# Kernel optimization log

Hardware: AMD Instinct MI355X
Metric: run time of the kernel (lower is better)

Reference implementation:

```python
import jax, jax.numpy as jnp
import numpy as np

D_MODEL = 256
NHEAD = 8
D_HEAD = D_MODEL // NHEAD
DIM_FF = 1024
B, L = 4, 16384
LN_EPS = 1e-5


def _layernorm(x, g, b):
    mu = jnp.mean(x, axis=-1, keepdims=True)
    var = jnp.mean((x - mu) ** 2, axis=-1, keepdims=True)
    return (x - mu) * jax.lax.rsqrt(var + LN_EPS) * g + b


def _phi(x):
    # elu(x) + 1
    return jnp.where(x > 0, x + 1.0, jnp.exp(x))


def setup_inputs() -> dict:
    key = jax.random.key(0)
    ks = jax.random.split(key, 16)
    s_in = 1.0 / np.sqrt(D_MODEL)
    s_ff = 1.0 / np.sqrt(DIM_FF)
    inp = {
        "x": jax.random.normal(ks[0], (B, L, D_MODEL), dtype=jnp.float32),
        "Wq": jax.random.normal(ks[1], (D_MODEL, D_MODEL), dtype=jnp.float32) * s_in,
        "bq": jnp.zeros((D_MODEL,), jnp.float32),
        "Wk": jax.random.normal(ks[2], (D_MODEL, D_MODEL), dtype=jnp.float32) * s_in,
        "bk": jnp.zeros((D_MODEL,), jnp.float32),
        "Wv": jax.random.normal(ks[3], (D_MODEL, D_MODEL), dtype=jnp.float32) * s_in,
        "bv": jnp.zeros((D_MODEL,), jnp.float32),
        "Wo": jax.random.normal(ks[4], (D_MODEL, D_MODEL), dtype=jnp.float32) * s_in,
        "bo": jnp.zeros((D_MODEL,), jnp.float32),
        "W1": jax.random.normal(ks[5], (D_MODEL, DIM_FF), dtype=jnp.float32) * s_in,
        "b1": jnp.zeros((DIM_FF,), jnp.float32),
        "W2": jax.random.normal(ks[6], (DIM_FF, D_MODEL), dtype=jnp.float32) * s_ff,
        "b2": jnp.zeros((D_MODEL,), jnp.float32),
        "ln1_g": jnp.ones((D_MODEL,), jnp.float32),
        "ln1_b": jnp.zeros((D_MODEL,), jnp.float32),
        "ln2_g": jnp.ones((D_MODEL,), jnp.float32),
        "ln2_b": jnp.zeros((D_MODEL,), jnp.float32),
    }
    return inp


def reference(x, Wq, bq, Wk, bk, Wv, bv, Wo, bo, W1, b1, W2, b2, ln1_g, ln1_b, ln2_g, ln2_b):
    Bq, Lq, _ = x.shape
    q = (x @ Wq + bq).reshape(Bq, Lq, NHEAD, D_HEAD)
    k = (x @ Wk + bk).reshape(Bq, Lq, NHEAD, D_HEAD)
    v = (x @ Wv + bv).reshape(Bq, Lq, NHEAD, D_HEAD)
    q_phi = _phi(q)
    k_phi = _phi(k)
    # kv: [B, H, d, e]
    kv = jnp.einsum("blhd,blhe->bhde", k_phi, v)
    k_sum = k_phi.sum(axis=1)  # [B, H, d]
    z = 1.0 / (jnp.einsum("blhd,bhd->blh", q_phi, k_sum) + 1e-6)
    out = jnp.einsum("blhd,bhde,blh->blhe", q_phi, kv, z)
    out = out.reshape(Bq, Lq, D_MODEL) @ Wo + bo
    x = _layernorm(x + out, ln1_g, ln1_b)
    ff = jax.nn.relu(x @ W1 + b1) @ W2 + b2
    x = _layernorm(x + ff, ln2_g, ln2_b)
    return x
```

## Files before the change

### kernel.cpp

```cpp
#include <hip/hip_runtime.h>
#include <hip/hip_bf16.h>
#include <math.h>

#define NTOK   65536
#define L_SEQ  16384

typedef __bf16 bf16_t;
typedef bf16_t bf16x8 __attribute__((ext_vector_type(8)));
typedef bf16_t bf16x4 __attribute__((ext_vector_type(4)));
typedef float  f32x4  __attribute__((ext_vector_type(4)));

__device__ inline float phi_f(float x) { return x > 0.f ? x + 1.f : __expf(x); }

__device__ inline float quad_sum(float v) {
    v += __shfl_xor(v, 1);
    v += __shfl_xor(v, 2);
    v += __shfl_xor(v, 4);
    v += __shfl_xor(v, 8);
    return v;
}

__device__ inline float ld_any(const void* p, size_t i, int f32) {
    return f32 ? ((const float*)p)[i] : (float)((const bf16_t*)p)[i];
}

__device__ inline void async_copy16(const bf16_t* g, bf16_t* l) {
    __builtin_amdgcn_global_load_lds(
        (const __attribute__((address_space(1))) unsigned int*)g,
        (__attribute__((address_space(3))) unsigned int*)l, 16, 0, 0);
}

__device__ inline void stage_swz(const bf16_t* __restrict__ g, bf16_t* lds,
                                 int tid, int nslot, int ulog2, int rowstride) {
    const int umask = (1 << ulog2) - 1;
    for (int s = tid; s < nslot; s += 256) {
        int n = s >> ulog2, j = s & umask;
        int u = j ^ (n & umask);
        async_copy16(g + (size_t)n * rowstride + u * 8, lds + (size_t)s * 8);
    }
}

__device__ inline bf16x8 rd_swz(const bf16_t* lds, int n, int u, int ulog2) {
    int j = u ^ (n & ((1 << ulog2) - 1));
    return *(const bf16x8*)&lds[(((size_t)n << ulog2) + j) * 8];
}

__device__ inline void stage_w2ff(const bf16_t* __restrict__ W2_t, int ch,
                                  bf16_t* lds, int tid) {
    for (int S = tid; S < 1024; S += 256) {
        int r = S >> 3, phys = S & 7;
        int u = phys ^ (r & 7);
        int n = ((u >> 2) << 7) + r;
        int ks = u & 3;
        async_copy16(W2_t + (size_t)n * 1024 + ch * 32 + ks * 8, lds + (size_t)S * 8);
    }
}

__device__ inline bf16x8 rd_w2ff(const bf16_t* lds, int n, int quad) {
    int r = n & 127;
    int u = ((n >> 7) << 2) + quad;
    int phys = u ^ (r & 7);
    return *(const bf16x8*)&lds[(size_t)(r * 8 + phys) * 8];
}

__device__ inline void ld_afrags(const bf16_t* __restrict__ tile, int row, int q8,
                                 bf16x8 a[8]) {
#pragma unroll
    for (int kk = 0; kk < 8; ++kk)
        a[kk] = *(const bf16x8*)&tile[(size_t)row * 256 + kk * 32 + q8];
}

__global__ __launch_bounds__(256) void k_detect(const void* __restrict__ xraw,
                                                int* __restrict__ flag) {
    __shared__ int bad;
    if (threadIdx.x == 0) bad = 0;
    __syncthreads();
    const bf16_t* xb = (const bf16_t*)xraw;
    int mybad = 0;
#pragma unroll
    for (int j = 0; j < 16; ++j) {
        float v = fabsf((float)xb[threadIdx.x + 256 * j]);
        if (!(v <= 1000.f)) mybad = 1;
    }
    if (mybad) atomicOr(&bad, 1);
    __syncthreads();
    if (threadIdx.x == 0) *flag = bad;
}

__global__ __launch_bounds__(256) void k_convert(const void* __restrict__ xraw,
                                                 const int* __restrict__ flag,
                                                 bf16_t* __restrict__ xbf) {
    const int f = *flag;
    size_t i = ((size_t)blockIdx.x * 256 + threadIdx.x) * 4;
    if (f) {
        f32x4 v = *(const f32x4*)((const float*)xraw + i);
        bf16x4 o;
#pragma unroll
        for (int j = 0; j < 4; ++j) o[j] = (bf16_t)v[j];
        *(bf16x4*)&xbf[i] = o;
    } else {
        *(bf16x4*)&xbf[i] = *(const bf16x4*)((const bf16_t*)xraw + i);
    }
}

__global__ __launch_bounds__(256) void k_prep(
    const void* __restrict__ Wq, const void* __restrict__ Wk,
    const void* __restrict__ Wv, const void* __restrict__ Wo,
    const void* __restrict__ W1, const void* __restrict__ W2,
    const void* __restrict__ bq, const void* __restrict__ bk,
    const void* __restrict__ bv, const void* __restrict__ bo,
    const void* __restrict__ b1, const void* __restrict__ b2,
    const void* __restrict__ g1, const void* __restrict__ be1,
    const void* __restrict__ g2, const void* __restrict__ be2,
    const int* __restrict__ flag,
    bf16_t* __restrict__ Wqkv_t, bf16_t* __restrict__ Wo_t,
    bf16_t* __restrict__ W1_t, bf16_t* __restrict__ W2_t,
    bf16_t* __restrict__ pbuf, float* __restrict__ kvbuf) {
    const int f = *flag;
    int idx = blockIdx.x * 256 + threadIdx.x;
    if (idx < 196608) {
        int n = idx >> 8, k = idx & 255;
        float v;
        if (n < 256)      v = ld_any(Wq, k * 256 + n, f);
        else if (n < 512) v = ld_any(Wk, k * 256 + (n - 256), f);
        else              v = ld_any(Wv, k * 256 + (n - 512), f);
        Wqkv_t[idx] = (bf16_t)v;
    } else if (idx < 262144) {
        int i = idx - 196608; int n = i >> 8, k = i & 255;
        Wo_t[i] = (bf16_t)ld_any(Wo, k * 256 + n, f);
    } else if (idx < 524288) {
        int i = idx - 262144; int n = i >> 8, k = i & 255;
        W1_t[i] = (bf16_t)ld_any(W1, k * 1024 + n, f);
    } else if (idx < 786432) {
        int i = idx - 524288; int n = i >> 10, k = i & 1023;
        W2_t[i] = (bf16_t)ld_any(W2, k * 256 + n, f);
    } else if (idx < 820224) {
        kvbuf[idx - 786432] = 0.f;
    } else if (idx < 823552) {
        int i = idx - 820224;
        float v;
        if (i < 256)        v = ld_any(bq, i, f);
        else if (i < 512)   v = ld_any(bk, i - 256, f);
        else if (i < 768)   v = ld_any(bv, i - 512, f);
        else if (i < 1024)  v = ld_any(bo, i - 768, f);
        else if (i < 2048)  v = ld_any(b1, i - 1024, f);
        else if (i < 2304)  v = ld_any(b2, i - 2048, f);
        else if (i < 2560)  v = ld_any(g1, i - 2304, f);
        else if (i < 2816)  v = ld_any(be1, i - 2560, f);
        else if (i < 3072)  v = ld_any(g2, i - 2816, f);
        else                v = ld_any(be2, i - 3072, f);
        pbuf[i] = (bf16_t)v;
    }
}

__global__ __launch_bounds__(256, 4) void k_qkv(
    const bf16_t* __restrict__ x, const bf16_t* __restrict__ Wqkv_t,
    const bf16_t* __restrict__ pbuf,
    bf16_t* __restrict__ q_phi, bf16_t* __restrict__ k_phi,
    bf16_t* __restrict__ v_out) {
    const int mt = blockIdx.x, nt = blockIdx.y;
    const int tid = threadIdx.x, wave = tid >> 6, lane = tid & 63;
    const int l15 = lane & 15, quad = lane >> 4, q8 = quad * 8;
    __shared__ __align__(16) bf16_t bs[128 * 256];
    const int m0 = mt * 64;
    bf16x8 a[8];
    ld_afrags(x + (size_t)m0 * 256, wave * 16 + l15, q8, a);
    stage_swz(Wqkv_t + (size_t)nt * 128 * 256, bs, tid, 4096, 5, 256);
    __syncthreads();
    f32x4 acc[8] = {};
#pragma unroll
    for (int kk = 0; kk < 8; ++kk) {
#pragma unroll
        for (int s = 0; s < 8; ++s) {
            bf16x8 b = rd_swz(bs, s * 16 + l15, kk * 4 + quad, 5);
            acc[s] = __builtin_amdgcn_mfma_f32_16x16x32_bf16(a[kk], b, acc[s], 0, 0, 0);
        }
    }
#pragma unroll
    for (int s = 0; s < 8; ++s) {
        int ng = nt * 128 + s * 16 + l15;
        bf16_t* dst = ng < 256 ? q_phi : (ng < 512 ? k_phi : v_out);
        int nl = ng & 255;
        float bias = (float)pbuf[(ng < 256 ? 0 : (ng < 512 ? 256 : 512)) + nl];
#pragma unroll
        for (int r = 0; r < 4; ++r) {
            int m = m0 + wave * 16 + quad * 4 + r;
            float val = acc[s][r] + bias;
            if (ng < 512) val = phi_f(val);
            dst[(size_t)m * 256 + nl] = (bf16_t)val;
        }
    }
}

__global__ __launch_bounds__(256) void k_kvsum(
    const bf16_t* __restrict__ k_phi, const bf16_t* __restrict__ v_in,
    float* __restrict__ kvbuf) {
    const int bid = blockIdx.x;
    const int bh = bid >> 6, ck = bid & 63;
    const int b = bh >> 3, h = bh & 7;
    const int tid = threadIdx.x;
    __shared__ float ks[32][33], vs[32][33];
    const size_t base = ((size_t)b * L_SEQ + ck * 256) * 256 + h * 32;
    const int row = tid >> 3, c4 = (tid & 7) * 4;
    const int d = row, e4 = c4;
    float acc[4] = {}, ksacc = 0.f;
    for (int it = 0; it < 8; ++it) {
        bf16x4 kk4 = *(const bf16x4*)&k_phi[base + (size_t)(it * 32 + row) * 256 + c4];
        bf16x4 vv4 = *(const bf16x4*)&v_in[base + (size_t)(it * 32 + row) * 256 + c4];
#pragma unroll
        for (int j = 0; j < 4; ++j) { ks[row][c4 + j] = (float)kk4[j]; vs[row][c4 + j] = (float)vv4[j]; }
        __syncthreads();
#pragma unroll
        for (int ii = 0; ii < 32; ++ii) {
            float kd = ks[ii][d];
            ksacc += kd;
#pragma unroll
            for (int j = 0; j < 4; ++j) acc[j] += kd * vs[ii][e4 + j];
        }
        __syncthreads();
    }
    float* kvdst = kvbuf + (size_t)bh * 1056;
#pragma unroll
    for (int j = 0; j < 4; ++j) atomicAdd(&kvdst[(e4 + j) * 32 + d], acc[j]);
    if ((tid & 7) == 0) atomicAdd(&kvdst[1024 + d], ksacc);
}

__global__ __launch_bounds__(256) void k_kvprep(const float* __restrict__ kvbuf,
                                                bf16_t* __restrict__ kvbf) {
    int idx = blockIdx.x * 256 + threadIdx.x;
    int bh = idx >> 8, r4 = (idx & 255) * 4;
    f32x4 v = *(const f32x4*)&kvbuf[(size_t)bh * 1056 + r4];
    bf16x4 o;
#pragma unroll
    for (int j = 0; j < 4; ++j) o[j] = (bf16_t)v[j];
    *(bf16x4*)&kvbf[(size_t)bh * 1024 + r4] = o;
}

__global__ __launch_bounds__(256, 3) void k_attn_wo_ln1(
    const bf16_t* __restrict__ q_phi, const bf16_t* __restrict__ kvbf,
    const float* __restrict__ kvbuf, const bf16_t* __restrict__ Wo_t,
    const bf16_t* __restrict__ pbuf, const void* __restrict__ xraw,
    const int* __restrict__ flag, bf16_t* __restrict__ x1) {
    const int f = *flag;
    const int mt = blockIdx.x;
    const int tid = threadIdx.x, wave = tid >> 6, lane = tid & 63;
    const int l15 = lane & 15, quad = lane >> 4, q8 = quad * 8;
    __shared__ __align__(16) bf16_t sm0[8192];
    __shared__ __align__(16) bf16_t sm1[16896];
    const int m0 = mt * 64;
    const int b = m0 >> 14;
    bf16x8 a[8];
    ld_afrags(q_phi + (size_t)m0 * 256, wave * 16 + l15, q8, a);
    stage_swz(Wo_t, sm0, tid, 1024, 5, 256);
    bf16_t* hs = sm1 + wave * (16 * 264);
    const bf16_t* kvb = kvbf + (size_t)b * 8192;
    const float*  ksb = kvbuf + (size_t)b * 8448;
#pragma unroll
    for (int h = 0; h < 8; ++h) {
        f32x4 ks0 = *(const f32x4*)&ksb[h * 1056 + 1024 + q8];
        f32x4 ks1 = *(const f32x4*)&ksb[h * 1056 + 1024 + q8 + 4];
        float den = 0.f;
#pragma unroll
        for (int j = 0; j < 4; ++j) den += (float)a[h][j] * ks0[j];
#pragma unroll
        for (int j = 0; j < 4; ++j) den += (float)a[h][4 + j] * ks1[j];
        den += __shfl_xor(den, 16);
        den += __shfl_xor(den, 32);
        float z = 1.f / (den + 1e-6f);
        float zr[4];
#pragma unroll
        for (int r = 0; r < 4; ++r) zr[r] = __shfl(z, quad * 4 + r, 16);
        bf16x8 b0 = *(const bf16x8*)&kvb[h * 1024 + l15 * 32 + q8];
        bf16x8 b1 = *(const bf16x8*)&kvb[h * 1024 + (16 + l15) * 32 + q8];
        f32x4 at0 = {}, at1 = {};
        at0 = __builtin_amdgcn_mfma_f32_16x16x32_bf16(a[h], b0, at0, 0, 0, 0);
        at1 = __builtin_amdgcn_mfma_f32_16x16x32_bf16(a[h], b1, at1, 0, 0, 0);
#pragma unroll
        for (int r = 0; r < 4; ++r) {
            hs[(quad * 4 + r) * 264 + h * 32 + l15]      = (bf16_t)(at0[r] * zr[r]);
            hs[(quad * 4 + r) * 264 + h * 32 + 16 + l15] = (bf16_t)(at1[r] * zr[r]);
        }
    }
    bf16x8 a2[8];
#pragma unroll
    for (int kk = 0; kk < 8; ++kk)
        a2[kk] = *(const bf16x8*)&hs[l15 * 264 + kk * 32 + q8];
    __syncthreads();
    f32x4 acc[16] = {};
    for (int nc = 0; nc < 8; ++nc) {
        if (nc < 7) stage_swz(Wo_t + (size_t)(nc + 1) * 32 * 256,
                              (nc & 1) ? sm0 : sm1, tid, 1024, 5, 256);
        const bf16_t* buf = (nc & 1) ? sm1 : sm0;
#pragma unroll
        for (int kk = 0; kk < 8; ++kk) {
#pragma unroll
            for (int s = 0; s < 2; ++s) {
                bf16x8 bb = rd_swz(buf, s * 16 + l15, kk * 4 + quad, 5);
                acc[nc * 2 + s] = __builtin_amdgcn_mfma_f32_16x16x32_bf16(a2[kk], bb, acc[nc * 2 + s], 0, 0, 0);
            }
        }
        __syncthreads();
    }
    float s1[4] = {}, s2[4] = {};
#pragma unroll
    for (int s = 0; s < 16; ++s) {
        int n = s * 16 + l15;
        float bias = (float)pbuf[768 + n];
#pragma unroll
        for (int r = 0; r < 4; ++r) {
            int m = m0 + wave * 16 + quad * 4 + r;
            float val = acc[s][r] + bias + ld_any(xraw, (size_t)m * 256 + n, f);
            acc[s][r] = val;
            s1[r] += val; s2[r] += val * val;
        }
    }
#pragma unroll
    for (int r = 0; r < 4; ++r) {
        float ts = quad_sum(s1[r]), ts2 = quad_sum(s2[r]);
        float mu = ts * (1.f / 256.f);
        float rs = rsqrtf(ts2 * (1.f / 256.f) - mu * mu + 1e-5f);
        s1[r] = mu; s2[r] = rs;
    }
#pragma unroll
    for (int s = 0; s < 16; ++s) {
        int n = s * 16 + l15;
        float gn = (float)pbuf[2304 + n], bn = (float)pbuf[2560 + n];
#pragma unroll
        for (int r = 0; r < 4; ++r) {
            int m = m0 + wave * 16 + quad * 4 + r;
            x1[(size_t)m * 256 + n] = (bf16_t)((acc[s][r] - s1[r]) * s2[r] * gn + bn);
        }
    }
}

__global__ __launch_bounds__(256, 3) void k_ff_ln2(
    const bf16_t* __restrict__ x1, const bf16_t* __restrict__ W1_t,
    const bf16_t* __restrict__ W2_t, const bf16_t* __restrict__ pbuf,
    const int* __restrict__ flag, void* __restrict__ out) {
    const int f32o = *flag;
    const int mt = blockIdx.x;
    const int tid = threadIdx.x, wave = tid >> 6, lane = tid & 63;
    const int l15 = lane & 15, quad = lane >> 4, q8 = quad * 8;
    __shared__ __align__(16) bf16_t w1s[2][8192];
    __shared__ __align__(16) bf16_t w2s[2][8192];
    __shared__ __align__(16) bf16_t hs[4][16][40];
    const int m0 = mt * 64;
    bf16x8 a[8];
    ld_afrags(x1 + (size_t)m0 * 256, wave * 16 + l15, q8, a);
    stage_swz(W1_t, w1s[0], tid, 1024, 5, 256);
    stage_w2ff(W2_t, 0, w2s[0], tid);
    __syncthreads();
    f32x4 acc[16] = {};
    for (int ch = 0; ch < 32; ++ch) {
        const int cur = ch & 1;
        if (ch < 31) {
            stage_swz(W1_t + (size_t)(ch + 1) * 32 * 256, w1s[cur ^ 1], tid, 1024, 5, 256);
            stage_w2ff(W2_t, ch + 1, w2s[cur ^ 1], tid);
        }
        f32x4 hacc[2] = {};
#pragma unroll
        for (int kk = 0; kk < 8; ++kk) {
#pragma unroll
            for (int s = 0; s < 2; ++s) {
                bf16x8 b = rd_swz(w1s[cur], s * 16 + l15, kk * 4 + quad, 5);
                hacc[s] = __builtin_amdgcn_mfma_f32_16x16x32_bf16(a[kk], b, hacc[s], 0, 0, 0);
            }
        }
#pragma unroll
        for (int s = 0; s < 2; ++s) {
            float bias = (float)pbuf[1024 + ch * 32 + s * 16 + l15];
#pragma unroll
            for (int r = 0; r < 4; ++r) {
                float val = hacc[s][r] + bias;
                hs[wave][quad * 4 + r][s * 16 + l15] = (bf16_t)(val > 0.f ? val : 0.f);
            }
        }
        bf16x8 a2 = *(const bf16x8*)&hs[wave][l15][q8];
#pragma unroll
        for (int s = 0; s < 16; ++s) {
            bf16x8 b0 = rd_w2ff(w2s[cur], s * 16 + l15, quad);
            acc[s] = __builtin_amdgcn_mfma_f32_16x16x32_bf16(a2, b0, acc[s], 0, 0, 0);
        }
        __syncthreads();
    }
    float s1[4] = {}, s2[4] = {};
#pragma unroll
    for (int s = 0; s < 16; ++s) {
        int n = s * 16 + l15;
        float bias = (float)pbuf[2048 + n];
#pragma unroll
        for (int r = 0; r < 4; ++r) {
            int m = m0 + wave * 16 + quad * 4 + r;
            float val = acc[s][r] + bias + (float)x1[(size_t)m * 256 + n];
            acc[s][r] = val;
            s1[r] += val; s2[r] += val * val;
        }
    }
#pragma unroll
    for (int r = 0; r < 4; ++r) {
        float ts = quad_sum(s1[r]), ts2 = quad_sum(s2[r]);
        float mu = ts * (1.f / 256.f);
        float rs = rsqrtf(ts2 * (1.f / 256.f) - mu * mu + 1e-5f);
        s1[r] = mu; s2[r] = rs;
    }
#pragma unroll
    for (int s = 0; s < 16; ++s) {
        int n = s * 16 + l15;
        float gn = (float)pbuf[2816 + n], bn = (float)pbuf[3072 + n];
#pragma unroll
        for (int r = 0; r < 4; ++r) {
            int m = m0 + wave * 16 + quad * 4 + r;
            float val = (acc[s][r] - s1[r]) * s2[r] * gn + bn;
            if (f32o) ((float*)out)[(size_t)m * 256 + n] = val;
            else      ((bf16_t*)out)[(size_t)m * 256 + n] = (bf16_t)val;
        }
    }
}

extern "C" void kernel_launch(void* const* d_in, const int* in_sizes, int n_in,
                              void* d_out, int out_size, void* d_ws, size_t ws_size,
                              hipStream_t stream) {
    char* ws = (char*)d_ws;
    int*    flag   = (int*)ws;
    bf16_t* xbf    = (bf16_t*)(ws + 256);
    bf16_t* Wqkv_t = (bf16_t*)(ws + 33554688);
    bf16_t* Wo_t   = (bf16_t*)(ws + 33947904);
    bf16_t* W1_t   = (bf16_t*)(ws + 34078976);
    bf16_t* W2_t   = (bf16_t*)(ws + 34603264);
    bf16_t* pbuf   = (bf16_t*)(ws + 35127552);
    float*  kvbuf  = (float*)(ws + 35134208);
    bf16_t* bufQ   = (bf16_t*)(ws + 35269376);
    bf16_t* bufK   = bufQ + (size_t)NTOK * 256;
    bf16_t* bufV   = bufK + (size_t)NTOK * 256;
    bf16_t* kvbf   = bufV;
    bf16_t* bufX1  = bufQ;

    k_detect<<<1, 256, 0, stream>>>(d_in[0], flag);
    k_convert<<<16384, 256, 0, stream>>>(d_in[0], flag, xbf);
    k_prep<<<3217, 256, 0, stream>>>(d_in[1], d_in[3], d_in[5], d_in[7],
                                     d_in[9], d_in[11],
                                     d_in[2], d_in[4], d_in[6], d_in[8],
                                     d_in[10], d_in[12],
                                     d_in[13], d_in[14], d_in[15], d_in[16],
                                     flag, Wqkv_t, Wo_t, W1_t, W2_t, pbuf, kvbuf);
    k_qkv<<<dim3(1024, 6), 256, 0, stream>>>(xbf, Wqkv_t, pbuf, bufQ, bufK, bufV);
    k_kvsum<<<2048, 256, 0, stream>>>(bufK, bufV, kvbuf);
    k_kvprep<<<32, 256, 0, stream>>>(kvbuf, kvbf);
    k_attn_wo_ln1<<<1024, 256, 0, stream>>>(bufQ, kvbf, kvbuf, Wo_t, pbuf,
                                            d_in[0], flag, bufX1);
    k_ff_ln2<<<1024, 256, 0, stream>>>(bufX1, W1_t, W2_t, pbuf, flag, d_out);
}
```

Measured before the change: 432.3 us.

## Double rows per wave in FF kernel to reuse staged weight tiles

Each wave in the feed-forward+LN2 kernel now processes 32 rows instead of 16, so each block covers 128 tokens and the grid halves to 512 blocks. Every W1/W2 fragment read from shared memory feeds two MFMAs, halving the total weight staging and LDS traffic per token. The cost is doubled accumulator registers (launch bounds lowered from 3 to 2 waves-per-SIMD hint) and fewer blocks, which lowers occupancy and on a 256-CU part leaves the grid with only about two blocks per CU.

```diff
diff --git a/kernel.cpp b/kernel.cpp
--- a/kernel.cpp
+++ b/kernel.cpp
@@ -333,7 +333,7 @@
     }
 }
 
-__global__ __launch_bounds__(256, 3) void k_ff_ln2(
+__global__ __launch_bounds__(256, 2) void k_ff_ln2(
     const bf16_t* __restrict__ x1, const bf16_t* __restrict__ W1_t,
     const bf16_t* __restrict__ W2_t, const bf16_t* __restrict__ pbuf,
     const int* __restrict__ flag, void* __restrict__ out) {
@@ -343,27 +343,29 @@
     const int l15 = lane & 15, quad = lane >> 4, q8 = quad * 8;
     __shared__ __align__(16) bf16_t w1s[2][8192];
     __shared__ __align__(16) bf16_t w2s[2][8192];
-    __shared__ __align__(16) bf16_t hs[4][16][40];
-    const int m0 = mt * 64;
-    bf16x8 a[8];
-    ld_afrags(x1 + (size_t)m0 * 256, wave * 16 + l15, q8, a);
+    __shared__ __align__(16) bf16_t hs[4][2][16][40];
+    const int m0 = mt * 128 + wave * 32;
+    bf16x8 a[2][8];
+    ld_afrags(x1 + (size_t)m0 * 256, l15,      q8, a[0]);
+    ld_afrags(x1 + (size_t)m0 * 256, 16 + l15, q8, a[1]);
     stage_swz(W1_t, w1s[0], tid, 1024, 5, 256);
     stage_w2ff(W2_t, 0, w2s[0], tid);
     __syncthreads();
-    f32x4 acc[16] = {};
+    f32x4 acc[2][16] = {};
     for (int ch = 0; ch < 32; ++ch) {
         const int cur = ch & 1;
         if (ch < 31) {
             stage_swz(W1_t + (size_t)(ch + 1) * 32 * 256, w1s[cur ^ 1], tid, 1024, 5, 256);
             stage_w2ff(W2_t, ch + 1, w2s[cur ^ 1], tid);
         }
-        f32x4 hacc[2] = {};
+        f32x4 h0[2] = {}, h1[2] = {};
 #pragma unroll
         for (int kk = 0; kk < 8; ++kk) {
 #pragma unroll
             for (int s = 0; s < 2; ++s) {
                 bf16x8 b = rd_swz(w1s[cur], s * 16 + l15, kk * 4 + quad, 5);
-                hacc[s] = __builtin_amdgcn_mfma_f32_16x16x32_bf16(a[kk], b, hacc[s], 0, 0, 0);
+                h0[s] = __builtin_amdgcn_mfma_f32_16x16x32_bf16(a[0][kk], b, h0[s], 0, 0, 0);
+                h1[s] = __builtin_amdgcn_mfma_f32_16x16x32_bf16(a[1][kk], b, h1[s], 0, 0, 0);
             }
         }
 #pragma unroll
@@ -371,48 +373,55 @@
             float bias = (float)pbuf[1024 + ch * 32 + s * 16 + l15];
 #pragma unroll
             for (int r = 0; r < 4; ++r) {
-                float val = hacc[s][r] + bias;
-                hs[wave][quad * 4 + r][s * 16 + l15] = (bf16_t)(val > 0.f ? val : 0.f);
+                float v0 = h0[s][r] + bias;
+                float v1 = h1[s][r] + bias;
+                hs[wave][0][quad * 4 + r][s * 16 + l15] = (bf16_t)(v0 > 0.f ? v0 : 0.f);
+                hs[wave][1][quad * 4 + r][s * 16 + l15] = (bf16_t)(v1 > 0.f ? v1 : 0.f);
             }
         }
-        bf16x8 a2 = *(const bf16x8*)&hs[wave][l15][q8];
+        bf16x8 a2_0 = *(const bf16x8*)&hs[wave][0][l15][q8];
+        bf16x8 a2_1 = *(const bf16x8*)&hs[wave][1][l15][q8];
 #pragma unroll
         for (int s = 0; s < 16; ++s) {
             bf16x8 b0 = rd_w2ff(w2s[cur], s * 16 + l15, quad);
-            acc[s] = __builtin_amdgcn_mfma_f32_16x16x32_bf16(a2, b0, acc[s], 0, 0, 0);
+            acc[0][s] = __builtin_amdgcn_mfma_f32_16x16x32_bf16(a2_0, b0, acc[0][s], 0, 0, 0);
+            acc[1][s] = __builtin_amdgcn_mfma_f32_16x16x32_bf16(a2_1, b0, acc[1][s], 0, 0, 0);
         }
         __syncthreads();
     }
-    float s1[4] = {}, s2[4] = {};
-#pragma unroll
-    for (int s = 0; s < 16; ++s) {
-        int n = s * 16 + l15;
-        float bias = (float)pbuf[2048 + n];
+#pragma unroll
+    for (int mm = 0; mm < 2; ++mm) {
+        float s1[4] = {}, s2[4] = {};
+#pragma unroll
+        for (int s = 0; s < 16; ++s) {
+            int n = s * 16 + l15;
+            float bias = (float)pbuf[2048 + n];
+#pragma unroll
+            for (int r = 0; r < 4; ++r) {
+                int m = m0 + mm * 16 + quad * 4 + r;
+                float val = acc[mm][s][r] + bias + (float)x1[(size_t)m * 256 + n];
+                acc[mm][s][r] = val;
+                s1[r] += val; s2[r] += val * val;
+            }
+        }
 #pragma unroll
         for (int r = 0; r < 4; ++r) {
-            int m = m0 + wave * 16 + quad * 4 + r;
-            float val = acc[s][r] + bias + (float)x1[(size_t)m * 256 + n];
-            acc[s][r] = val;
-            s1[r] += val; s2[r] += val * val;
-        }
-    }
-#pragma unroll
-    for (int r = 0; r < 4; ++r) {
-        float ts = quad_sum(s1[r]), ts2 = quad_sum(s2[r]);
-        float mu = ts * (1.f / 256.f);
-        float rs = rsqrtf(ts2 * (1.f / 256.f) - mu * mu + 1e-5f);
-        s1[r] = mu; s2[r] = rs;
-    }
-#pragma unroll
-    for (int s = 0; s < 16; ++s) {
-        int n = s * 16 + l15;
-        float gn = (float)pbuf[2816 + n], bn = (float)pbuf[3072 + n];
-#pragma unroll
-        for (int r = 0; r < 4; ++r) {
-            int m = m0 + wave * 16 + quad * 4 + r;
-            float val = (acc[s][r] - s1[r]) * s2[r] * gn + bn;
-            if (f32o) ((float*)out)[(size_t)m * 256 + n] = val;
-            else      ((bf16_t*)out)[(size_t)m * 256 + n] = (bf16_t)val;
+            float ts = quad_sum(s1[r]), ts2 = quad_sum(s2[r]);
+            float mu = ts * (1.f / 256.f);
+            float rs = rsqrtf(ts2 * (1.f / 256.f) - mu * mu + 1e-5f);
+            s1[r] = mu; s2[r] = rs;
+        }
+#pragma unroll
+        for (int s = 0; s < 16; ++s) {
+            int n = s * 16 + l15;
+            float gn = (float)pbuf[2816 + n], bn = (float)pbuf[3072 + n];
+#pragma unroll
+            for (int r = 0; r < 4; ++r) {
+                int m = m0 + mm * 16 + quad * 4 + r;
+                float val = (acc[mm][s][r] - s1[r]) * s2[r] * gn + bn;
+                if (f32o) ((float*)out)[(size_t)m * 256 + n] = val;
+                else      ((bf16_t*)out)[(size_t)m * 256 + n] = (bf16_t)val;
+            }
         }
     }
 }
@@ -448,5 +457,5 @@
     k_kvprep<<<32, 256, 0, stream>>>(kvbuf, kvbf);
     k_attn_wo_ln1<<<1024, 256, 0, stream>>>(bufQ, kvbf, kvbuf, Wo_t, pbuf,
                                             d_in[0], flag, bufX1);
-    k_ff_ln2<<<1024, 256, 0, stream>>>(bufX1, W1_t, W2_t, pbuf, flag, d_out);
-}
+    k_ff_ln2<<<512, 256, 0, stream>>>(bufX1, W1_t, W2_t, pbuf, flag, d_out);
+}
```

Measured after the change: 409.0 us. 1.06x faster.
